# Kernel tuning notes

Measured on AMD Instinct MI355X. Metric: run time of the kernel, lower is better.

The kernel has to match this reference:

```python
import jax, jax.numpy as jnp
import numpy as np

N, E, FEAT, EMB, HID, V, EA, G = 10000, 250000, 16, 32, 32, 12, 9, 64
TEMP = 1.0


def setup_inputs() -> dict:
    key = jax.random.key(0)
    ks = jax.random.split(key, 20)
    p = lambda k, shp: jax.random.normal(k, shp, dtype=jnp.float32) * 0.05
    return {
        "x": jax.random.normal(ks[0], (N, FEAT), dtype=jnp.float32),
        "edge_attr": jax.random.normal(ks[1], (E, EA), dtype=jnp.float32),
        "edge_index": jax.random.randint(ks[2], (2, E), 0, N),
        "batch": jnp.sort(jax.random.randint(ks[3], (N,), 0, G)),
        # conv1 edge MLP: Linear(EA,32) -> ReLU -> Linear(32, FEAT*EMB)
        "nn1_w1": p(ks[4], (EA, 32)), "nn1_b1": p(ks[5], (32,)),
        "nn1_w2": p(ks[6], (32, FEAT * EMB)), "nn1_b2": p(ks[7], (FEAT * EMB,)),
        "root1": p(ks[8], (FEAT, EMB)), "bias1": p(ks[9], (EMB,)),
        # conv2 edge MLP: Linear(EA,32) -> ReLU -> Linear(32, EMB*HID)
        "nn2_w1": p(ks[10], (EA, 32)), "nn2_b1": p(ks[11], (32,)),
        "nn2_w2": p(ks[12], (32, EMB * HID)), "nn2_b2": p(ks[13], (EMB * HID,)),
        "root2": p(ks[14], (EMB, HID)), "bias2": p(ks[15], (HID,)),
        "lin_w": p(ks[16], (HID, V)), "lin_b": p(ks[17], (V,)),
    }


def _segment_mean(vals, ids, num_segments):
    s = jax.ops.segment_sum(vals, ids, num_segments=num_segments)
    cnt = jax.ops.segment_sum(jnp.ones((vals.shape[0],), vals.dtype), ids,
                              num_segments=num_segments)
    return s / jnp.maximum(cnt, 1.0)[:, None]


def _nnconv(h, edge_attr, src, dst, w1, b1, w2, b2, root, bias, din, dout):
    # edge MLP -> per-edge weight matrix [E, din, dout]
    we = (jax.nn.relu(edge_attr @ w1 + b1) @ w2 + b2).reshape(-1, din, dout)
    msg = jnp.einsum('ei,eio->eo', h[src], we)      # gather + per-edge matmul
    agg = _segment_mean(msg, dst, h.shape[0])       # scatter-mean to targets
    return agg + h @ root + bias                    # root weight + bias


def reference(x, edge_attr, edge_index, batch,
              nn1_w1, nn1_b1, nn1_w2, nn1_b2, root1, bias1,
              nn2_w1, nn2_b1, nn2_w2, nn2_b2, root2, bias2,
              lin_w, lin_b):
    src, dst = edge_index[0], edge_index[1]
    h = jax.nn.relu(_nnconv(x, edge_attr, src, dst,
                            nn1_w1, nn1_b1, nn1_w2, nn1_b2, root1, bias1,
                            FEAT, EMB))
    h = jax.nn.relu(_nnconv(h, edge_attr, src, dst,
                            nn2_w1, nn2_b1, nn2_w2, nn2_b2, root2, bias2,
                            EMB, HID))
    pooled = _segment_mean(h, batch, G)             # global_mean_pool [G, HID]
    logits = (pooled @ lin_w + lin_b) / TEMP
    return jax.nn.log_softmax(logits, axis=1)
```

## Files before the change

kernel.cpp:

```cpp
#include <hip/hip_runtime.h>
#include <hip/hip_bf16.h>
#include <stdint.h>

#define NN 10000
#define NE 250000
#define FEAT 16
#define EMB 32
#define HID 32
#define NV 12
#define EAD 9
#define NG 64
#define EPB 128
#define NCH 25

__device__ __forceinline__ uint32_t bf16rne(float f) {
    uint32_t u = __float_as_uint(f);
    return (u + 0x7fffu + ((u >> 16) & 1u)) >> 16;
}
__device__ __forceinline__ float blo(uint32_t p) { return __uint_as_float(p << 16); }
__device__ __forceinline__ float bhi(uint32_t p) { return __uint_as_float(p & 0xffff0000u); }

__global__ void edge_stats_kernel(const int* __restrict__ src,
                                  const int* __restrict__ dst,
                                  int* __restrict__ histS,
                                  int* __restrict__ histD) {
    int e = blockIdx.x * blockDim.x + threadIdx.x;
    if (e >= NE) return;
    atomicAdd(&histS[src[e]], 1);
    atomicAdd(&histD[dst[e]], 1);
}

__global__ __launch_bounds__(1024) void scan_kernel(const int* __restrict__ hist,
                                                    int* __restrict__ rowStart,
                                                    int* __restrict__ cursor) {
    __shared__ int part[1024];
    int t = threadIdx.x;
    int base = t * 10;
    int local[10];
    int s = 0;
#pragma unroll
    for (int i = 0; i < 10; ++i) {
        int v = (base + i < NN) ? hist[base + i] : 0;
        local[i] = s;
        s += v;
    }
    part[t] = s;
    __syncthreads();
    for (int off = 1; off < 1024; off <<= 1) {
        int v = (t >= off) ? part[t - off] : 0;
        __syncthreads();
        part[t] += v;
        __syncthreads();
    }
    int pre = (t == 0) ? 0 : part[t - 1];
#pragma unroll
    for (int i = 0; i < 10; ++i) {
        if (base + i < NN) {
            int rs = pre + local[i];
            rowStart[base + i] = rs;
            cursor[base + i] = rs;
        }
    }
    if (t == 1023) rowStart[NN] = part[1023];
}

__global__ void scatter_kernel(const float* __restrict__ ea,
                               const int* __restrict__ src,
                               const int* __restrict__ dst,
                               int* __restrict__ cursorS,
                               float* __restrict__ ea_p,
                               int* __restrict__ src_s,
                               int* __restrict__ dst_s) {
    int e = blockIdx.x * blockDim.x + threadIdx.x;
    if (e >= NE) return;
    int sv = src[e];
    int pos = atomicAdd(&cursorS[sv], 1);
    src_s[pos] = sv;
    dst_s[pos] = dst[e];
#pragma unroll
    for (int j = 0; j < 12; ++j)
        ea_p[(size_t)pos * 12 + j] = (j < EAD) ? ea[(size_t)e * EAD + j] : 0.f;
}

template <int DIN>
__global__ __launch_bounds__(256) void computeQ_pack_kernel(
    const float* __restrict__ h,
    const float* __restrict__ w2,
    uint32_t* __restrict__ Qp)
{
    int t = threadIdx.x;
    int o = t & 31;
    int kk = (blockIdx.y * 256 + t) >> 5;
    float w0[DIN], w1r[DIN];
    const float* wa = w2 + (size_t)(2 * kk) * (DIN * 32) + o;
    const float* wb = w2 + (size_t)(2 * kk + 1) * (DIN * 32) + o;
#pragma unroll
    for (int i = 0; i < DIN; ++i) { w0[i] = wa[i * 32]; w1r[i] = wb[i * 32]; }

    int n0 = blockIdx.x * NCH;
    for (int j = 0; j < NCH; ++j) {
        int n = n0 + j;
        const float* hn = h + (size_t)n * DIN;
        float s0 = 0.f, s1 = 0.f;
#pragma unroll
        for (int i = 0; i < DIN; ++i) {
            float hv = hn[i];
            s0 += hv * w0[i];
            s1 += hv * w1r[i];
        }
        Qp[((size_t)n * 16 + kk) * 32 + o] = (bf16rne(s1) << 16) | bf16rne(s0);
    }
}

template <int DIN>
__global__ void computeQbias_kernel(const float* __restrict__ h,
                                    const float* __restrict__ b2,
                                    float* __restrict__ Qb) {
    int idx = blockIdx.x * blockDim.x + threadIdx.x;
    if (idx >= NN * 32) return;
    int o = idx & 31;
    int n = idx >> 5;
    const float* hn = h + (size_t)n * DIN;
    float s = 0.f;
#pragma unroll
    for (int i = 0; i < DIN; ++i) s += hn[i] * b2[i * 32 + o];
    Qb[idx] = s;
}

__global__ __launch_bounds__(256) void edge_agg_kernel(
    const float* __restrict__ ea_p,
    const int* __restrict__ src_s,
    const int* __restrict__ dst_s,
    const float* __restrict__ w1,
    const float* __restrict__ b1,
    const uint32_t* __restrict__ Qp,
    const float* __restrict__ Qb,
    float* __restrict__ agg)
{
    __shared__ float s_hid[8][32];
    int t = threadIdx.x;
    int o = t & 31;
    int slot = t >> 5;

    float w1r[12];
#pragma unroll
    for (int j = 0; j < 12; ++j) w1r[j] = (j < EAD) ? w1[j * 32 + o] : 0.f;
    float b1r = b1[o];

    int base = blockIdx.x * EPB;
    int eend = min(base + EPB, NE);
    for (int e = base + slot; e < eend; e += 8) {
        const float4* eav = (const float4*)(ea_p + (size_t)e * 12);
        float4 a0 = eav[0], a1 = eav[1], a2 = eav[2];
        float hs = b1r;
        hs += a0.x * w1r[0] + a0.y * w1r[1] + a0.z * w1r[2] + a0.w * w1r[3];
        hs += a1.x * w1r[4] + a1.y * w1r[5] + a1.z * w1r[6] + a1.w * w1r[7];
        hs += a2.x * w1r[8];
        float hd = fmaxf(hs, 0.f);

        s_hid[slot][o] = hd;
        __builtin_amdgcn_wave_barrier();

        int sv = src_s[e];
        const uint32_t* q = Qp + (size_t)sv * 512 + o;
        float m = Qb[(size_t)sv * 32 + o];
        const float4* hq = (const float4*)(&s_hid[slot][0]);
#pragma unroll
        for (int c = 0; c < 8; ++c) {
            float4 hv = hq[c];
            uint32_t qa  = q[(2 * c) * 32];
            uint32_t qb2 = q[(2 * c + 1) * 32];
            m += hv.x * blo(qa) + hv.y * bhi(qa)
               + hv.z * blo(qb2) + hv.w * bhi(qb2);
        }
        atomicAdd(&agg[(size_t)dst_s[e] * 32 + o], m);
        __builtin_amdgcn_wave_barrier();
    }
}

template <int DIN>
__global__ void node_update_kernel(const float* __restrict__ agg,
                                   const int* __restrict__ histD,
                                   const float* __restrict__ hin,
                                   const float* __restrict__ root,
                                   const float* __restrict__ bias,
                                   float* __restrict__ hout,
                                   float* __restrict__ pooled,
                                   const int* __restrict__ batch,
                                   float* __restrict__ gcnt)
{
    int idx = blockIdx.x * blockDim.x + threadIdx.x;
    if (idx >= NN * 32) return;
    int o = idx & 31;
    int n = idx >> 5;
    float s = bias[o] + agg[idx] / fmaxf((float)histD[n], 1.0f);
    const float* h = hin + (size_t)n * DIN;
#pragma unroll
    for (int i = 0; i < DIN; ++i) s += h[i] * root[i * 32 + o];
    s = fmaxf(s, 0.f);
    hout[idx] = s;
    if (pooled) {
        int g = batch[n];
        atomicAdd(&pooled[g * 32 + o], s);
        if (o == 0) atomicAdd(&gcnt[g], 1.0f);
    }
}

__global__ void final_kernel(const float* __restrict__ pooled,
                             const float* __restrict__ gcnt,
                             const float* __restrict__ lin_w,
                             const float* __restrict__ lin_b,
                             float* __restrict__ out) {
    int g = threadIdx.x;
    if (g >= NG) return;
    float inv = 1.0f / fmaxf(gcnt[g], 1.0f);
    float p[HID];
#pragma unroll
    for (int h = 0; h < HID; ++h) p[h] = pooled[g * HID + h] * inv;
    float logits[NV];
    float mx = -1e30f;
#pragma unroll
    for (int v = 0; v < NV; ++v) {
        float s = lin_b[v];
#pragma unroll
        for (int h = 0; h < HID; ++h) s += p[h] * lin_w[h * NV + v];
        logits[v] = s;
        mx = fmaxf(mx, s);
    }
    float se = 0.f;
#pragma unroll
    for (int v = 0; v < NV; ++v) se += expf(logits[v] - mx);
    float lse = mx + logf(se);
#pragma unroll
    for (int v = 0; v < NV; ++v) out[g * NV + v] = logits[v] - lse;
}

extern "C" void kernel_launch(void* const* d_in, const int* in_sizes, int n_in,
                              void* d_out, int out_size, void* d_ws, size_t ws_size,
                              hipStream_t stream) {
    const float* x        = (const float*)d_in[0];
    const float* ea       = (const float*)d_in[1];
    const int*   eidx     = (const int*)d_in[2];
    const int*   batch    = (const int*)d_in[3];
    const float* nn1_w1   = (const float*)d_in[4];
    const float* nn1_b1   = (const float*)d_in[5];
    const float* nn1_w2   = (const float*)d_in[6];
    const float* nn1_b2   = (const float*)d_in[7];
    const float* root1    = (const float*)d_in[8];
    const float* bias1    = (const float*)d_in[9];
    const float* nn2_w1   = (const float*)d_in[10];
    const float* nn2_b1   = (const float*)d_in[11];
    const float* nn2_w2   = (const float*)d_in[12];
    const float* nn2_b2   = (const float*)d_in[13];
    const float* root2    = (const float*)d_in[14];
    const float* bias2    = (const float*)d_in[15];
    const float* lin_w    = (const float*)d_in[16];
    const float* lin_b    = (const float*)d_in[17];
    float* out = (float*)d_out;

    const int* src = eidx;
    const int* dst = eidx + NE;

    char* base = (char*)d_ws;
    uint32_t* Qp   = (uint32_t*)base;
    float* ea_p    = (float*)(Qp + (size_t)NN * 512);
    float* Qb      = ea_p + (size_t)NE * 12;
    float* h1      = Qb + (size_t)NN * 32;
    float* h2      = h1 + (size_t)NN * 32;
    int*   src_s   = (int*)(h2 + (size_t)NN * 32);
    int*   dst_s   = src_s + NE;
    int*   rowS    = dst_s + NE;
    int*   curS    = rowS + NN + 1;
    int*   histS   = curS + NN;
    int*   histD   = histS + NN;
    float* pooled  = (float*)(histD + NN);
    float* gcnt    = pooled + NG * 32;
    float* agg     = gcnt + NG;
    size_t zero_bytes = ((size_t)NN * 2 + NG * 32 + NG + (size_t)NN * 32) * 4;

    hipMemsetAsync(histS, 0, zero_bytes, stream);

    edge_stats_kernel<<<(NE + 255) / 256, 256, 0, stream>>>(src, dst, histS, histD);
    scan_kernel<<<1, 1024, 0, stream>>>(histS, rowS, curS);
    scatter_kernel<<<(NE + 255) / 256, 256, 0, stream>>>(ea, src, dst, curS,
                                                         ea_p, src_s, dst_s);

    const int edge_grid = (NE + EPB - 1) / EPB;
    dim3 qgrid(NN / NCH, 2);

    computeQ_pack_kernel<FEAT><<<qgrid, 256, 0, stream>>>(x, nn1_w2, Qp);
    computeQbias_kernel<FEAT><<<(NN * 32) / 256, 256, 0, stream>>>(x, nn1_b2, Qb);
    edge_agg_kernel<<<edge_grid, 256, 0, stream>>>(ea_p, src_s, dst_s,
                                                   nn1_w1, nn1_b1, Qp, Qb, agg);
    node_update_kernel<FEAT><<<(NN * 32) / 256, 256, 0, stream>>>(
        agg, histD, x, root1, bias1, h1, nullptr, nullptr, nullptr);

    hipMemsetAsync(agg, 0, (size_t)NN * 32 * sizeof(float), stream);
    computeQ_pack_kernel<EMB><<<qgrid, 256, 0, stream>>>(h1, nn2_w2, Qp);
    computeQbias_kernel<EMB><<<(NN * 32) / 256, 256, 0, stream>>>(h1, nn2_b2, Qb);
    edge_agg_kernel<<<edge_grid, 256, 0, stream>>>(ea_p, src_s, dst_s,
                                                   nn2_w1, nn2_b1, Qp, Qb, agg);
    node_update_kernel<EMB><<<(NN * 32) / 256, 256, 0, stream>>>(
        agg, histD, h1, root2, bias2, h2, pooled, batch, gcnt);

    final_kernel<<<1, 64, 0, stream>>>(pooled, gcnt, lin_w, lin_b, out);
}
```

Baseline: 279.2 us.

## Sort edges by destination and fuse aggregation with node update per node

Edges are now bucketed by destination instead of source. A wave per node accumulates messages in registers and then applies the mean, root weight, bias, ReLU and pooling directly. This replaces the per-edge float atomics into agg, the agg memset, and the separate node update kernel. The cost is that Qp gathers by source become random rather than sorted, and per-node work is uneven because degrees vary.

```diff
diff --git a/kernel.cpp b/kernel.cpp
--- a/kernel.cpp
+++ b/kernel.cpp
@@ -10,7 +10,6 @@
 #define NV 12
 #define EAD 9
 #define NG 64
-#define EPB 128
 #define NCH 25
 
 __device__ __forceinline__ uint32_t bf16rne(float f) {
@@ -20,13 +19,10 @@
 __device__ __forceinline__ float blo(uint32_t p) { return __uint_as_float(p << 16); }
 __device__ __forceinline__ float bhi(uint32_t p) { return __uint_as_float(p & 0xffff0000u); }
 
-__global__ void edge_stats_kernel(const int* __restrict__ src,
-                                  const int* __restrict__ dst,
-                                  int* __restrict__ histS,
+__global__ void edge_stats_kernel(const int* __restrict__ dst,
                                   int* __restrict__ histD) {
     int e = blockIdx.x * blockDim.x + threadIdx.x;
     if (e >= NE) return;
-    atomicAdd(&histS[src[e]], 1);
     atomicAdd(&histD[dst[e]], 1);
 }
 
@@ -67,19 +63,17 @@
 __global__ void scatter_kernel(const float* __restrict__ ea,
                                const int* __restrict__ src,
                                const int* __restrict__ dst,
-                               int* __restrict__ cursorS,
-                               float* __restrict__ ea_p,
-                               int* __restrict__ src_s,
-                               int* __restrict__ dst_s) {
+                               int* __restrict__ cursorD,
+                               float* __restrict__ ea_d,
+                               int* __restrict__ src_d) {
     int e = blockIdx.x * blockDim.x + threadIdx.x;
     if (e >= NE) return;
-    int sv = src[e];
-    int pos = atomicAdd(&cursorS[sv], 1);
-    src_s[pos] = sv;
-    dst_s[pos] = dst[e];
+    int dv = dst[e];
+    int pos = atomicAdd(&cursorD[dv], 1);
+    src_d[pos] = src[e];
 #pragma unroll
     for (int j = 0; j < 12; ++j)
-        ea_p[(size_t)pos * 12 + j] = (j < EAD) ? ea[(size_t)e * EAD + j] : 0.f;
+        ea_d[(size_t)pos * 12 + j] = (j < EAD) ? ea[(size_t)e * EAD + j] : 0.f;
 }
 
 template <int DIN>
@@ -127,30 +121,41 @@
     Qb[idx] = s;
 }
 
-__global__ __launch_bounds__(256) void edge_agg_kernel(
-    const float* __restrict__ ea_p,
-    const int* __restrict__ src_s,
-    const int* __restrict__ dst_s,
+template <int DIN, bool POOL>
+__global__ __launch_bounds__(256) void conv_fused_kernel(
+    const float* __restrict__ ea_d,
+    const int* __restrict__ src_d,
+    const int* __restrict__ rowD,
     const float* __restrict__ w1,
     const float* __restrict__ b1,
     const uint32_t* __restrict__ Qp,
     const float* __restrict__ Qb,
-    float* __restrict__ agg)
+    const float* __restrict__ hin,
+    const float* __restrict__ root,
+    const float* __restrict__ bias,
+    float* __restrict__ hout,
+    float* __restrict__ pooled,
+    const int* __restrict__ batch,
+    float* __restrict__ gcnt)
 {
-    __shared__ float s_hid[8][32];
+    __shared__ float s_hid[4][2][32];
     int t = threadIdx.x;
-    int o = t & 31;
-    int slot = t >> 5;
-
-    float w1r[12];
-#pragma unroll
-    for (int j = 0; j < 12; ++j) w1r[j] = (j < EAD) ? w1[j * 32 + o] : 0.f;
+    int wv = t >> 6;
+    int lane = t & 63;
+    int half = lane >> 5;
+    int o = lane & 31;
+
+    float w1r[EAD];
+#pragma unroll
+    for (int j = 0; j < EAD; ++j) w1r[j] = w1[j * 32 + o];
     float b1r = b1[o];
 
-    int base = blockIdx.x * EPB;
-    int eend = min(base + EPB, NE);
-    for (int e = base + slot; e < eend; e += 8) {
-        const float4* eav = (const float4*)(ea_p + (size_t)e * 12);
+    int n = blockIdx.x * 4 + wv;
+    int beg = rowD[n], end = rowD[n + 1];
+
+    float acc = 0.f;
+    for (int e = beg + half; e < end; e += 2) {
+        const float4* eav = (const float4*)(ea_d + (size_t)e * 12);
         float4 a0 = eav[0], a1 = eav[1], a2 = eav[2];
         float hs = b1r;
         hs += a0.x * w1r[0] + a0.y * w1r[1] + a0.z * w1r[2] + a0.w * w1r[3];
@@ -158,13 +163,13 @@
         hs += a2.x * w1r[8];
         float hd = fmaxf(hs, 0.f);
 
-        s_hid[slot][o] = hd;
+        s_hid[wv][half][o] = hd;
         __builtin_amdgcn_wave_barrier();
 
-        int sv = src_s[e];
+        int sv = src_d[e];
         const uint32_t* q = Qp + (size_t)sv * 512 + o;
         float m = Qb[(size_t)sv * 32 + o];
-        const float4* hq = (const float4*)(&s_hid[slot][0]);
+        const float4* hq = (const float4*)(&s_hid[wv][half][0]);
 #pragma unroll
         for (int c = 0; c < 8; ++c) {
             float4 hv = hq[c];
@@ -173,36 +178,26 @@
             m += hv.x * blo(qa) + hv.y * bhi(qa)
                + hv.z * blo(qb2) + hv.w * bhi(qb2);
         }
-        atomicAdd(&agg[(size_t)dst_s[e] * 32 + o], m);
+        acc += m;
         __builtin_amdgcn_wave_barrier();
     }
-}
-
-template <int DIN>
-__global__ void node_update_kernel(const float* __restrict__ agg,
-                                   const int* __restrict__ histD,
-                                   const float* __restrict__ hin,
-                                   const float* __restrict__ root,
-                                   const float* __restrict__ bias,
-                                   float* __restrict__ hout,
-                                   float* __restrict__ pooled,
-                                   const int* __restrict__ batch,
-                                   float* __restrict__ gcnt)
-{
-    int idx = blockIdx.x * blockDim.x + threadIdx.x;
-    if (idx >= NN * 32) return;
-    int o = idx & 31;
-    int n = idx >> 5;
-    float s = bias[o] + agg[idx] / fmaxf((float)histD[n], 1.0f);
-    const float* h = hin + (size_t)n * DIN;
-#pragma unroll
-    for (int i = 0; i < DIN; ++i) s += h[i] * root[i * 32 + o];
+
+    acc += __shfl_xor(acc, 32);
+
+    float inv = 1.0f / fmaxf((float)(end - beg), 1.0f);
+    float s = acc * inv + bias[o];
+    const float* hrow = hin + (size_t)n * DIN;
+#pragma unroll
+    for (int i = 0; i < DIN; ++i) s += hrow[i] * root[i * 32 + o];
     s = fmaxf(s, 0.f);
-    hout[idx] = s;
-    if (pooled) {
-        int g = batch[n];
-        atomicAdd(&pooled[g * 32 + o], s);
-        if (o == 0) atomicAdd(&gcnt[g], 1.0f);
+
+    if (half == 0) {
+        hout[(size_t)n * 32 + o] = s;
+        if (POOL) {
+            int g = batch[n];
+            atomicAdd(&pooled[g * 32 + o], s);
+            if (o == 0) atomicAdd(&gcnt[g], 1.0f);
+        }
     }
 }
 
@@ -263,45 +258,39 @@
 
     char* base = (char*)d_ws;
     uint32_t* Qp   = (uint32_t*)base;
-    float* ea_p    = (float*)(Qp + (size_t)NN * 512);
-    float* Qb      = ea_p + (size_t)NE * 12;
+    float* ea_d    = (float*)(Qp + (size_t)NN * 512);
+    float* Qb      = ea_d + (size_t)NE * 12;
     float* h1      = Qb + (size_t)NN * 32;
     float* h2      = h1 + (size_t)NN * 32;
-    int*   src_s   = (int*)(h2 + (size_t)NN * 32);
-    int*   dst_s   = src_s + NE;
-    int*   rowS    = dst_s + NE;
-    int*   curS    = rowS + NN + 1;
-    int*   histS   = curS + NN;
-    int*   histD   = histS + NN;
+    int*   src_d   = (int*)(h2 + (size_t)NN * 32);
+    int*   rowD    = src_d + NE;
+    int*   curD    = rowD + NN + 1;
+    int*   histD   = curD + NN;
     float* pooled  = (float*)(histD + NN);
     float* gcnt    = pooled + NG * 32;
-    float* agg     = gcnt + NG;
-    size_t zero_bytes = ((size_t)NN * 2 + NG * 32 + NG + (size_t)NN * 32) * 4;
-
-    hipMemsetAsync(histS, 0, zero_bytes, stream);
-
-    edge_stats_kernel<<<(NE + 255) / 256, 256, 0, stream>>>(src, dst, histS, histD);
-    scan_kernel<<<1, 1024, 0, stream>>>(histS, rowS, curS);
-    scatter_kernel<<<(NE + 255) / 256, 256, 0, stream>>>(ea, src, dst, curS,
-                                                         ea_p, src_s, dst_s);
-
-    const int edge_grid = (NE + EPB - 1) / EPB;
+    size_t zero_bytes = ((size_t)NN + NG * 32 + NG) * 4;
+
+    hipMemsetAsync(histD, 0, zero_bytes, stream);
+
+    edge_stats_kernel<<<(NE + 255) / 256, 256, 0, stream>>>(dst, histD);
+    scan_kernel<<<1, 1024, 0, stream>>>(histD, rowD, curD);
+    scatter_kernel<<<(NE + 255) / 256, 256, 0, stream>>>(ea, src, dst, curD,
+                                                         ea_d, src_d);
+
     dim3 qgrid(NN / NCH, 2);
+    const int conv_grid = NN / 4;
 
     computeQ_pack_kernel<FEAT><<<qgrid, 256, 0, stream>>>(x, nn1_w2, Qp);
     computeQbias_kernel<FEAT><<<(NN * 32) / 256, 256, 0, stream>>>(x, nn1_b2, Qb);
-    edge_agg_kernel<<<edge_grid, 256, 0, stream>>>(ea_p, src_s, dst_s,
-                                                   nn1_w1, nn1_b1, Qp, Qb, agg);
-    node_update_kernel<FEAT><<<(NN * 32) / 256, 256, 0, stream>>>(
-        agg, histD, x, root1, bias1, h1, nullptr, nullptr, nullptr);
-
-    hipMemsetAsync(agg, 0, (size_t)NN * 32 * sizeof(float), stream);
+    conv_fused_kernel<FEAT, false><<<conv_grid, 256, 0, stream>>>(
+        ea_d, src_d, rowD, nn1_w1, nn1_b1, Qp, Qb,
+        x, root1, bias1, h1, nullptr, nullptr, nullptr);
+
     computeQ_pack_kernel<EMB><<<qgrid, 256, 0, stream>>>(h1, nn2_w2, Qp);
     computeQbias_kernel<EMB><<<(NN * 32) / 256, 256, 0, stream>>>(h1, nn2_b2, Qb);
-    edge_agg_kernel<<<edge_grid, 256, 0, stream>>>(ea_p, src_s, dst_s,
-                                                   nn2_w1, nn2_b1, Qp, Qb, agg);
-    node_update_kernel<EMB><<<(NN * 32) / 256, 256, 0, stream>>>(
-        agg, histD, h1, root2, bias2, h2, pooled, batch, gcnt);
+    conv_fused_kernel<EMB, true><<<conv_grid, 256, 0, stream>>>(
+        ea_d, src_d, rowD, nn2_w1, nn2_b1, Qp, Qb,
+        h1, root2, bias2, h2, pooled, batch, gcnt);
 
     final_kernel<<<1, 64, 0, stream>>>(pooled, gcnt, lin_w, lin_b, out);
 }
```

New measurement: 289.4 us. +3.7%, slower.

## Fuse Q-bias into Q pack, fuse layer-1 node update into Q2 compute

Applied to the files above, without the earlier changes.

Folds the per-node bias projection into the Q packing kernel, and merges the layer-1 node update (mean, root, bias, ReLU) into the layer-2 Q computation through shared memory. The second node update becomes a pooling kernel that no longer writes h2. Separate agg buffers replace the mid-pipeline memset, so the whole workspace is cleared once. This removes several launches and a round trip of intermediate data, but the node update is recomputed for each blockIdx.y and the kk==0 warp does extra bias work serially.

```diff
diff --git a/kernel.cpp b/kernel.cpp
--- a/kernel.cpp
+++ b/kernel.cpp
@@ -86,7 +86,9 @@
 __global__ __launch_bounds__(256) void computeQ_pack_kernel(
     const float* __restrict__ h,
     const float* __restrict__ w2,
-    uint32_t* __restrict__ Qp)
+    const float* __restrict__ b2,
+    uint32_t* __restrict__ Qp,
+    float* __restrict__ Qb)
 {
     int t = threadIdx.x;
     int o = t & 31;
@@ -109,22 +111,81 @@
             s1 += hv * w1r[i];
         }
         Qp[((size_t)n * 16 + kk) * 32 + o] = (bf16rne(s1) << 16) | bf16rne(s0);
-    }
-}
-
-template <int DIN>
-__global__ void computeQbias_kernel(const float* __restrict__ h,
-                                    const float* __restrict__ b2,
-                                    float* __restrict__ Qb) {
-    int idx = blockIdx.x * blockDim.x + threadIdx.x;
-    if (idx >= NN * 32) return;
-    int o = idx & 31;
-    int n = idx >> 5;
-    const float* hn = h + (size_t)n * DIN;
-    float s = 0.f;
-#pragma unroll
-    for (int i = 0; i < DIN; ++i) s += hn[i] * b2[i * 32 + o];
-    Qb[idx] = s;
+        if (kk == 0) {
+            float sb = 0.f;
+#pragma unroll
+            for (int i = 0; i < DIN; ++i) sb += hn[i] * b2[i * 32 + o];
+            Qb[(size_t)n * 32 + o] = sb;
+        }
+    }
+}
+
+__global__ __launch_bounds__(256) void computeQ2h_kernel(
+    const float* __restrict__ agg1,
+    const int* __restrict__ histD,
+    const float* __restrict__ x,
+    const float* __restrict__ root1,
+    const float* __restrict__ bias1,
+    const float* __restrict__ w2,
+    const float* __restrict__ b2,
+    float* __restrict__ h1out,
+    uint32_t* __restrict__ Qp,
+    float* __restrict__ Qb)
+{
+    __shared__ float s_x[NCH][17];
+    __shared__ float s_root[16][32];
+    __shared__ float s_h1[NCH][33];
+    __shared__ float s_bias[32];
+    __shared__ float s_deg[NCH];
+
+    int t = threadIdx.x;
+    int n0 = blockIdx.x * NCH;
+
+    for (int idx = t; idx < NCH * 16; idx += 256) {
+        int nl = idx >> 4, i = idx & 15;
+        s_x[nl][i] = x[(size_t)(n0 + nl) * 16 + i];
+    }
+    for (int idx = t; idx < 16 * 32; idx += 256)
+        s_root[idx >> 5][idx & 31] = root1[idx];
+    if (t < 32) s_bias[t] = bias1[t];
+    if (t < NCH) s_deg[t] = fmaxf((float)histD[n0 + t], 1.0f);
+    __syncthreads();
+
+    for (int idx = t; idx < NCH * 32; idx += 256) {
+        int nl = idx >> 5, i = idx & 31;
+        float v = agg1[(size_t)(n0 + nl) * 32 + i] / s_deg[nl] + s_bias[i];
+#pragma unroll
+        for (int j = 0; j < 16; ++j) v += s_x[nl][j] * s_root[j][i];
+        v = fmaxf(v, 0.f);
+        s_h1[nl][i] = v;
+        if (blockIdx.y == 0) h1out[(size_t)(n0 + nl) * 32 + i] = v;
+    }
+    __syncthreads();
+
+    int o = t & 31;
+    int kk = blockIdx.y * 8 + (t >> 5);
+    float w0[32], w1r[32];
+    const float* wa = w2 + (size_t)(2 * kk) * 1024 + o;
+    const float* wb = w2 + (size_t)(2 * kk + 1) * 1024 + o;
+#pragma unroll
+    for (int i = 0; i < 32; ++i) { w0[i] = wa[i * 32]; w1r[i] = wb[i * 32]; }
+
+    for (int j = 0; j < NCH; ++j) {
+        float s0 = 0.f, s1 = 0.f;
+#pragma unroll
+        for (int i = 0; i < 32; ++i) {
+            float hv = s_h1[j][i];
+            s0 += hv * w0[i];
+            s1 += hv * w1r[i];
+        }
+        Qp[((size_t)(n0 + j) * 16 + kk) * 32 + o] = (bf16rne(s1) << 16) | bf16rne(s0);
+        if (kk == 0) {
+            float sb = 0.f;
+#pragma unroll
+            for (int i = 0; i < 32; ++i) sb += s_h1[j][i] * b2[i * 32 + o];
+            Qb[(size_t)(n0 + j) * 32 + o] = sb;
+        }
+    }
 }
 
 __global__ __launch_bounds__(256) void edge_agg_kernel(
@@ -142,9 +203,9 @@
     int o = t & 31;
     int slot = t >> 5;
 
-    float w1r[12];
-#pragma unroll
-    for (int j = 0; j < 12; ++j) w1r[j] = (j < EAD) ? w1[j * 32 + o] : 0.f;
+    float w1r[EAD];
+#pragma unroll
+    for (int j = 0; j < EAD; ++j) w1r[j] = w1[j * 32 + o];
     float b1r = b1[o];
 
     int base = blockIdx.x * EPB;
@@ -178,30 +239,46 @@
     }
 }
 
-template <int DIN>
-__global__ void node_update_kernel(const float* __restrict__ agg,
-                                   const int* __restrict__ histD,
-                                   const float* __restrict__ hin,
-                                   const float* __restrict__ root,
-                                   const float* __restrict__ bias,
-                                   float* __restrict__ hout,
-                                   float* __restrict__ pooled,
-                                   const int* __restrict__ batch,
-                                   float* __restrict__ gcnt)
+__global__ __launch_bounds__(256) void pool_kernel(
+    const float* __restrict__ agg2,
+    const int* __restrict__ histD,
+    const float* __restrict__ h1,
+    const float* __restrict__ root2,
+    const float* __restrict__ bias2,
+    const int* __restrict__ batch,
+    float* __restrict__ pooled,
+    float* __restrict__ gcnt)
 {
-    int idx = blockIdx.x * blockDim.x + threadIdx.x;
-    if (idx >= NN * 32) return;
-    int o = idx & 31;
-    int n = idx >> 5;
-    float s = bias[o] + agg[idx] / fmaxf((float)histD[n], 1.0f);
-    const float* h = hin + (size_t)n * DIN;
-#pragma unroll
-    for (int i = 0; i < DIN; ++i) s += h[i] * root[i * 32 + o];
-    s = fmaxf(s, 0.f);
-    hout[idx] = s;
-    if (pooled) {
-        int g = batch[n];
-        atomicAdd(&pooled[g * 32 + o], s);
+    __shared__ float s_h1[NCH][33];
+    __shared__ float s_root[32][33];
+    __shared__ float s_bias[32];
+    __shared__ float s_deg[NCH];
+    __shared__ int s_batch[NCH];
+
+    int t = threadIdx.x;
+    int n0 = blockIdx.x * NCH;
+
+    for (int idx = t; idx < NCH * 32; idx += 256) {
+        int nl = idx >> 5, i = idx & 31;
+        s_h1[nl][i] = h1[(size_t)(n0 + nl) * 32 + i];
+    }
+    for (int idx = t; idx < 32 * 32; idx += 256)
+        s_root[idx >> 5][idx & 31] = root2[idx];
+    if (t < 32) s_bias[t] = bias2[t];
+    if (t < NCH) {
+        s_deg[t] = fmaxf((float)histD[n0 + t], 1.0f);
+        s_batch[t] = batch[n0 + t];
+    }
+    __syncthreads();
+
+    for (int idx = t; idx < NCH * 32; idx += 256) {
+        int nl = idx >> 5, o = idx & 31;
+        float v = agg2[(size_t)(n0 + nl) * 32 + o] / s_deg[nl] + s_bias[o];
+#pragma unroll
+        for (int i = 0; i < 32; ++i) v += s_h1[nl][i] * s_root[i][o];
+        v = fmaxf(v, 0.f);
+        int g = s_batch[nl];
+        atomicAdd(&pooled[g * 32 + o], v);
         if (o == 0) atomicAdd(&gcnt[g], 1.0f);
     }
 }
@@ -266,19 +343,19 @@
     float* ea_p    = (float*)(Qp + (size_t)NN * 512);
     float* Qb      = ea_p + (size_t)NE * 12;
     float* h1      = Qb + (size_t)NN * 32;
-    float* h2      = h1 + (size_t)NN * 32;
-    int*   src_s   = (int*)(h2 + (size_t)NN * 32);
+    float* agg1    = h1 + (size_t)NN * 32;
+    float* agg2    = agg1 + (size_t)NN * 32;
+    int*   histS   = (int*)(agg2 + (size_t)NN * 32);
+    int*   histD   = histS + NN;
+    float* pooled  = (float*)(histD + NN);
+    float* gcnt    = pooled + NG * 32;
+    size_t zero_bytes = ((size_t)NN * 64 + NN * 2 + NG * 32 + NG) * 4;
+    int*   src_s   = (int*)(gcnt + NG);
     int*   dst_s   = src_s + NE;
     int*   rowS    = dst_s + NE;
     int*   curS    = rowS + NN + 1;
-    int*   histS   = curS + NN;
-    int*   histD   = histS + NN;
-    float* pooled  = (float*)(histD + NN);
-    float* gcnt    = pooled + NG * 32;
-    float* agg     = gcnt + NG;
-    size_t zero_bytes = ((size_t)NN * 2 + NG * 32 + NG + (size_t)NN * 32) * 4;
-
-    hipMemsetAsync(histS, 0, zero_bytes, stream);
+
+    hipMemsetAsync(agg1, 0, zero_bytes, stream);
 
     edge_stats_kernel<<<(NE + 255) / 256, 256, 0, stream>>>(src, dst, histS, histD);
     scan_kernel<<<1, 1024, 0, stream>>>(histS, rowS, curS);
@@ -288,20 +365,18 @@
     const int edge_grid = (NE + EPB - 1) / EPB;
     dim3 qgrid(NN / NCH, 2);
 
-    computeQ_pack_kernel<FEAT><<<qgrid, 256, 0, stream>>>(x, nn1_w2, Qp);
-    computeQbias_kernel<FEAT><<<(NN * 32) / 256, 256, 0, stream>>>(x, nn1_b2, Qb);
+    computeQ_pack_kernel<FEAT><<<qgrid, 256, 0, stream>>>(x, nn1_w2, nn1_b2, Qp, Qb);
     edge_agg_kernel<<<edge_grid, 256, 0, stream>>>(ea_p, src_s, dst_s,
-                                                   nn1_w1, nn1_b1, Qp, Qb, agg);
-    node_update_kernel<FEAT><<<(NN * 32) / 256, 256, 0, stream>>>(
-        agg, histD, x, root1, bias1, h1, nullptr, nullptr, nullptr);
-
-    hipMemsetAsync(agg, 0, (size_t)NN * 32 * sizeof(float), stream);
-    computeQ_pack_kernel<EMB><<<qgrid, 256, 0, stream>>>(h1, nn2_w2, Qp);
-    computeQbias_kernel<EMB><<<(NN * 32) / 256, 256, 0, stream>>>(h1, nn2_b2, Qb);
+                                                   nn1_w1, nn1_b1, Qp, Qb, agg1);
+
+    computeQ2h_kernel<<<qgrid, 256, 0, stream>>>(
+        agg1, histD, x, root1, bias1, nn2_w2, nn2_b2, h1, Qp, Qb);
+
     edge_agg_kernel<<<edge_grid, 256, 0, stream>>>(ea_p, src_s, dst_s,
-                                                   nn2_w1, nn2_b1, Qp, Qb, agg);
-    node_update_kernel<EMB><<<(NN * 32) / 256, 256, 0, stream>>>(
-        agg, histD, h1, root2, bias2, h2, pooled, batch, gcnt);
+                                                   nn2_w1, nn2_b1, Qp, Qb, agg2);
+
+    pool_kernel<<<NN / NCH, 256, 0, stream>>>(
+        agg2, histD, h1, root2, bias2, batch, pooled, gcnt);
 
     final_kernel<<<1, 64, 0, stream>>>(pooled, gcnt, lin_w, lin_b, out);
 }
```

Measured after the change: 260.1 us. -6.8%, faster.
